# Optimization experiments

Measured on AMD Instinct MI355X. Metric: run time of the kernel, lower is better.

Reference implementation:

```python
import jax, jax.numpy as jnp
import numpy as np

D_NIBBLE = 16
NIBBLE_VALUES = 16
NUM_NIBBLES = 8


def _build_tables():
    num_entries = NIBBLE_VALUES * NIBBLE_VALUES * 2  # 512
    input_dim = 2 * D_NIBBLE + 2                     # 34
    W1 = np.zeros((input_dim, num_entries), dtype=np.float32)
    W2_sum = np.zeros((num_entries, D_NIBBLE), dtype=np.float32)
    W2_carry = np.zeros((num_entries, 2), dtype=np.float32)
    for a in range(NIBBLE_VALUES):
        for b in range(NIBBLE_VALUES):
            for c in range(2):
                k = a * 32 + b * 2 + c
                W1[a, k] = 1.0
                W1[D_NIBBLE + b, k] = 1.0
                W1[2 * D_NIBBLE + c, k] = 1.0
                total = a + b + c
                W2_sum[k, total % 16] = 1.0
                W2_carry[k, 1 if total >= 16 else 0] = 1.0
    return jnp.asarray(W1), jnp.asarray(W2_sum), jnp.asarray(W2_carry)


def setup_inputs() -> dict:
    key = jax.random.key(0)
    k1, k2 = jax.random.split(key)
    B = 32768
    a_nibbles = jax.random.uniform(k1, (B, NUM_NIBBLES, 32), dtype=jnp.float32)
    b_nibbles = jax.random.uniform(k2, (B, NUM_NIBBLES, 32), dtype=jnp.float32)
    W1, W2_sum, W2_carry = _build_tables()
    threshold = jnp.float32(2.5)
    return {"a_nibbles": a_nibbles, "b_nibbles": b_nibbles,
            "W1": W1, "W2_sum": W2_sum, "W2_carry": W2_carry,
            "threshold": threshold}


def reference(a_nibbles, b_nibbles, W1, W2_sum, W2_carry, threshold):
    # a_nibbles, b_nibbles: [B, 8, 32]; first 16 feats = value one-hot, rest = pos
    B = a_nibbles.shape[0]
    carry0 = jnp.zeros((B, 2), a_nibbles.dtype).at[:, 0].set(1.0)  # carry=0 one-hot
    a_steps = jnp.swapaxes(a_nibbles, 0, 1)  # [8, B, 32]
    b_steps = jnp.swapaxes(b_nibbles, 0, 1)

    def step(carry, ab):
        a, b = ab  # [B, 32] each
        x = jnp.concatenate([a[:, :D_NIBBLE], b[:, :D_NIBBLE], carry], axis=-1)  # [B,34]
        scores = x @ W1                                     # [B,512]
        weights = jax.nn.softmax((scores - threshold) * 10.0, axis=-1)
        result = weights @ W2_sum                           # [B,16]
        new_carry = weights @ W2_carry                      # [B,2]
        out = jnp.concatenate([result, a[:, D_NIBBLE:]], axis=-1)  # [B,32]
        return new_carry, out

    _, outs = jax.lax.scan(step, carry0, (a_steps, b_steps))  # outs: [8, B, 32]
    return jnp.swapaxes(outs, 0, 1)  # [B, 8, 32]
```

## Files before the change

### kernel.cpp

```cpp
#include <hip/hip_runtime.h>


#define LOG2E10 14.426950408889634f

#if __has_builtin(__builtin_amdgcn_exp2f)
#define EXP2F(x) __builtin_amdgcn_exp2f(x)
#else
#define EXP2F(x) exp2f(x)
#endif

#if __has_builtin(__builtin_amdgcn_rcpf)
#define RCPF(x) __builtin_amdgcn_rcpf(x)
#else
#define RCPF(x) (1.0f / (x))
#endif

#define EBZ(x) ebz[(x) + 12]

template <int CTRL>
__device__ __forceinline__ float qdpp(float x) {
    return __int_as_float(__builtin_amdgcn_update_dpp(
        0, __float_as_int(x), CTRL, 0xF, 0xF, true));
}

__global__ __launch_bounds__(256, 2) void AdditionFFN_kernel(
    const float4* __restrict__ A, const float4* __restrict__ Bv,
    float4* __restrict__ O, int nRows)
{
    const int T = threadIdx.x;
    const int c = T & 3;
    const int row = blockIdx.x * 64 + (T >> 2);
    if (row >= nRows) return;
    const float4* a4 = A + (size_t)row * 64;
    const float4* b4 = Bv + (size_t)row * 64;
    float4* o4 = O + (size_t)row * 64;

    float4 AV[8], BV[8], PV[8];
    #pragma unroll
    for (int s = 0; s < 8; ++s) {
        AV[s] = a4[s * 8 + c];
        BV[s] = b4[s * 8 + c];
        PV[s] = a4[s * 8 + 4 + c];
    }

    float ec0 = EXP2F(LOG2E10);
    float ec1 = 1.0f;

    #pragma unroll
    for (int s = 0; s < 8; ++s) {
        o4[s * 8 + 4 + c] = PV[s];

        const float4 av = AV[s], bv = BV[s];

        float ea_own[4] = { EXP2F(av.x * LOG2E10), EXP2F(av.y * LOG2E10),
                            EXP2F(av.z * LOG2E10), EXP2F(av.w * LOG2E10) };
        float eb_own[4] = { EXP2F(bv.x * LOG2E10), EXP2F(bv.y * LOG2E10),
                            EXP2F(bv.z * LOG2E10), EXP2F(bv.w * LOG2E10) };

        float ea[16];
        #pragma unroll
        for (int m = 0; m < 4; ++m) {
            ea[m]      = qdpp<0x00>(ea_own[m]);
            ea[4 + m]  = qdpp<0x55>(ea_own[m]);
            ea[8 + m]  = qdpp<0xAA>(ea_own[m]);
            ea[12 + m] = qdpp<0xFF>(ea_own[m]);
        }

        float ebr[4][4];
        #pragma unroll
        for (int m = 0; m < 4; ++m) {
            ebr[0][m] = eb_own[m];
            ebr[1][m] = qdpp<0x39>(eb_own[m]);
            ebr[2][m] = qdpp<0x4E>(eb_own[m]);
            ebr[3][m] = qdpp<0x93>(eb_own[m]);
        }

        float ebz[28];
        #pragma unroll
        for (int x = -12; x <= 15; ++x) {
            float vsh = ebr[(x >> 2) & 3][x & 3];
            bool keep;
            if (x >= 0 && x <= 3)  keep = true;
            else if (x < 0)        keep = (c >= ((3 - x) >> 2));
            else                   keep = (c <= ((15 - x) >> 2));
            EBZ(x) = keep ? vsh : 0.0f;
        }

        float ulo[5], uhi[5];
        #pragma unroll
        for (int i = 0; i < 5; ++i) {
            float acc = 0.0f;
            const int amax = (i + 11 < 15) ? (i + 11) : 15;
            #pragma unroll
            for (int a = 0; a <= amax; ++a) {
                acc = __builtin_fmaf(ea[a], EBZ(i - 1 - a), acc);
            }
            ulo[i] = acc;
        }
        #pragma unroll
        for (int i = 0; i < 5; ++i) {
            float acc = 0.0f;
            #pragma unroll
            for (int a = i; a < 16; ++a) {
                acc = __builtin_fmaf(ea[a], EBZ(i + 15 - a), acc);
            }
            uhi[i] = acc;
        }

        float sap = (ea_own[0] + ea_own[1]) + (ea_own[2] + ea_own[3]);
        sap += qdpp<0xB1>(sap);
        sap += qdpp<0x4E>(sap);
        float sbp = (eb_own[0] + eb_own[1]) + (eb_own[2] + eb_own[3]);
        sbp += qdpp<0xB1>(sbp);
        sbp += qdpp<0x4E>(sbp);
        const float E = ec0 + ec1;
        float Z = sap * sbp * E;
        float rZ = RCPF(Z);
        rZ = rZ * (2.0f - Z * rZ);

        float hi0p = (uhi[1] + uhi[2]) + (uhi[3] + uhi[4]);
        float phi = hi0p * E + ((c == 0) ? uhi[0] * ec1 : 0.0f);
        phi += qdpp<0xB1>(phi);
        phi += qdpp<0x4E>(phi);
        float carry1 = phi * rZ;
#if __has_builtin(__builtin_amdgcn_fmed3f)
        carry1 = __builtin_amdgcn_fmed3f(carry1, 0.0f, 1.0f);
#else
        carry1 = fminf(fmaxf(carry1, 0.0f), 1.0f);
#endif
        float carry0 = 1.0f - carry1;

        float vm1 = ulo[0] + uhi[0];
        float v0 = ulo[1] + uhi[1];
        float v1 = ulo[2] + uhi[2];
        float v2 = ulo[3] + uhi[3];
        float v3 = ulo[4] + uhi[4];
        float4 r;
        r.x = (v0 * ec0 + vm1 * ec1) * rZ;
        r.y = (v1 * ec0 + v0 * ec1) * rZ;
        r.z = (v2 * ec0 + v1 * ec1) * rZ;
        r.w = (v3 * ec0 + v2 * ec1) * rZ;
        o4[s * 8 + c] = r;

        ec0 = EXP2F(carry0 * LOG2E10);
        ec1 = EXP2F(carry1 * LOG2E10);
    }
}

extern "C" void kernel_launch(void* const* d_in, const int* in_sizes, int n_in,
                              void* d_out, int out_size, void* d_ws, size_t ws_size,
                              hipStream_t stream) {
    (void)n_in; (void)out_size; (void)d_ws; (void)ws_size;
    const int nRows = in_sizes[0] / 256;
    const float4* A  = (const float4*)d_in[0];
    const float4* Bv = (const float4*)d_in[1];
    float4* O = (float4*)d_out;
    int blocks = (nRows + 63) / 64;
    AdditionFFN_kernel<<<blocks, 256, 0, stream>>>(A, Bv, O, nRows);
}
```

Measured before the change: 112.8 us.

## Parallelize nibble steps across lanes, resolve carry chain with scalar scan

```diff
diff --git a/kernel.cpp b/kernel.cpp
--- a/kernel.cpp
+++ b/kernel.cpp
@@ -23,128 +23,144 @@
         0, __float_as_int(x), CTRL, 0xF, 0xF, true));
 }
 
-__global__ __launch_bounds__(256, 2) void AdditionFFN_kernel(
+template <int OFF>
+__device__ __forceinline__ float swz32(float x) {
+    return __int_as_float(__builtin_amdgcn_ds_swizzle(__float_as_int(x), OFF));
+}
+
+__global__ __launch_bounds__(256, 4) void AdditionFFN_kernel(
     const float4* __restrict__ A, const float4* __restrict__ Bv,
     float4* __restrict__ O, int nRows)
 {
     const int T = threadIdx.x;
-    const int c = T & 3;
-    const int row = blockIdx.x * 64 + (T >> 2);
+    const int r = T & 31;
+    const int c = r & 3;
+    const int s = r >> 2;
+    const int row = blockIdx.x * 8 + (T >> 5);
     if (row >= nRows) return;
     const float4* a4 = A + (size_t)row * 64;
     const float4* b4 = Bv + (size_t)row * 64;
     float4* o4 = O + (size_t)row * 64;
 
-    float4 AV[8], BV[8], PV[8];
+    const float4 av = a4[s * 8 + c];
+    const float4 bv = b4[s * 8 + c];
+    const float4 pv = a4[s * 8 + 4 + c];
+    o4[s * 8 + 4 + c] = pv;
+
+    float ea_own[4] = { EXP2F(av.x * LOG2E10), EXP2F(av.y * LOG2E10),
+                        EXP2F(av.z * LOG2E10), EXP2F(av.w * LOG2E10) };
+    float eb_own[4] = { EXP2F(bv.x * LOG2E10), EXP2F(bv.y * LOG2E10),
+                        EXP2F(bv.z * LOG2E10), EXP2F(bv.w * LOG2E10) };
+
+    float ea[16];
     #pragma unroll
-    for (int s = 0; s < 8; ++s) {
-        AV[s] = a4[s * 8 + c];
-        BV[s] = b4[s * 8 + c];
-        PV[s] = a4[s * 8 + 4 + c];
+    for (int m = 0; m < 4; ++m) {
+        ea[m]      = qdpp<0x00>(ea_own[m]);
+        ea[4 + m]  = qdpp<0x55>(ea_own[m]);
+        ea[8 + m]  = qdpp<0xAA>(ea_own[m]);
+        ea[12 + m] = qdpp<0xFF>(ea_own[m]);
     }
 
-    float ec0 = EXP2F(LOG2E10);
-    float ec1 = 1.0f;
+    float ebr[4][4];
+    #pragma unroll
+    for (int m = 0; m < 4; ++m) {
+        ebr[0][m] = eb_own[m];
+        ebr[1][m] = qdpp<0x39>(eb_own[m]);
+        ebr[2][m] = qdpp<0x4E>(eb_own[m]);
+        ebr[3][m] = qdpp<0x93>(eb_own[m]);
+    }
 
+    float ebz[28];
     #pragma unroll
-    for (int s = 0; s < 8; ++s) {
-        o4[s * 8 + 4 + c] = PV[s];
+    for (int x = -12; x <= 15; ++x) {
+        float vsh = ebr[(x >> 2) & 3][x & 3];
+        bool keep;
+        if (x >= 0 && x <= 3)  keep = true;
+        else if (x < 0)        keep = (c >= ((3 - x) >> 2));
+        else                   keep = (c <= ((15 - x) >> 2));
+        EBZ(x) = keep ? vsh : 0.0f;
+    }
 
-        const float4 av = AV[s], bv = BV[s];
+    float ulo[5], uhi[5];
+    #pragma unroll
+    for (int i = 0; i < 5; ++i) {
+        float acc = 0.0f;
+        const int amax = (i + 11 < 15) ? (i + 11) : 15;
+        #pragma unroll
+        for (int a = 0; a <= amax; ++a) {
+            acc = __builtin_fmaf(ea[a], EBZ(i - 1 - a), acc);
+        }
+        ulo[i] = acc;
+    }
+    #pragma unroll
+    for (int i = 0; i < 5; ++i) {
+        float acc = 0.0f;
+        #pragma unroll
+        for (int a = i; a < 16; ++a) {
+            acc = __builtin_fmaf(ea[a], EBZ(i + 15 - a), acc);
+        }
+        uhi[i] = acc;
+    }
 
-        float ea_own[4] = { EXP2F(av.x * LOG2E10), EXP2F(av.y * LOG2E10),
-                            EXP2F(av.z * LOG2E10), EXP2F(av.w * LOG2E10) };
-        float eb_own[4] = { EXP2F(bv.x * LOG2E10), EXP2F(bv.y * LOG2E10),
-                            EXP2F(bv.z * LOG2E10), EXP2F(bv.w * LOG2E10) };
+    float sap = (ea_own[0] + ea_own[1]) + (ea_own[2] + ea_own[3]);
+    sap += qdpp<0xB1>(sap);
+    sap += qdpp<0x4E>(sap);
+    float sbp = (eb_own[0] + eb_own[1]) + (eb_own[2] + eb_own[3]);
+    sbp += qdpp<0xB1>(sbp);
+    sbp += qdpp<0x4E>(sbp);
+    float Nm = sap * sbp;
+    float rN = RCPF(Nm);
+    rN = rN * (2.0f - Nm * rN);
 
-        float ea[16];
-        #pragma unroll
-        for (int m = 0; m < 4; ++m) {
-            ea[m]      = qdpp<0x00>(ea_own[m]);
-            ea[4 + m]  = qdpp<0x55>(ea_own[m]);
-            ea[8 + m]  = qdpp<0xAA>(ea_own[m]);
-            ea[12 + m] = qdpp<0xFF>(ea_own[m]);
-        }
+    float hi0p = (uhi[1] + uhi[2]) + (uhi[3] + uhi[4]);
+    hi0p += qdpp<0xB1>(hi0p);
+    hi0p += qdpp<0x4E>(hi0p);
+    float hs = hi0p * rN;
+    float ms = qdpp<0x00>(uhi[0]) * rN;
 
-        float ebr[4][4];
-        #pragma unroll
-        for (int m = 0; m < 4; ++m) {
-            ebr[0][m] = eb_own[m];
-            ebr[1][m] = qdpp<0x39>(eb_own[m]);
-            ebr[2][m] = qdpp<0x4E>(eb_own[m]);
-            ebr[3][m] = qdpp<0x93>(eb_own[m]);
-        }
+    float h0 = swz32<0x003>(hs), m0 = swz32<0x003>(ms);
+    float h1 = swz32<0x083>(hs), m1 = swz32<0x083>(ms);
+    float h2 = swz32<0x103>(hs), m2 = swz32<0x103>(ms);
+    float h3 = swz32<0x183>(hs), m3 = swz32<0x183>(ms);
+    float h4 = swz32<0x203>(hs), m4 = swz32<0x203>(ms);
+    float h5 = swz32<0x283>(hs), m5 = swz32<0x283>(ms);
+    float h6 = swz32<0x303>(hs), m6 = swz32<0x303>(ms);
+    float h7 = swz32<0x383>(hs), m7 = swz32<0x383>(ms);
 
-        float ebz[28];
-        #pragma unroll
-        for (int x = -12; x <= 15; ++x) {
-            float vsh = ebr[(x >> 2) & 3][x & 3];
-            bool keep;
-            if (x >= 0 && x <= 3)  keep = true;
-            else if (x < 0)        keep = (c >= ((3 - x) >> 2));
-            else                   keep = (c <= ((15 - x) >> 2));
-            EBZ(x) = keep ? vsh : 0.0f;
-        }
+    float c1 = 0.0f, wmine = 0.0f;
+#define CARRY_STEP(K, HK, MK)                                        \
+    {                                                                \
+        float e0 = EXP2F((1.0f - c1) * LOG2E10);                     \
+        float e1 = EXP2F(c1 * LOG2E10);                              \
+        float E = e0 + e1;                                           \
+        float rE = RCPF(E);                                          \
+        rE = rE * (2.0f - E * rE);                                   \
+        float w = e1 * rE;                                           \
+        if (s == K) wmine = w;                                       \
+        c1 = __builtin_fmaf(w, MK, HK);                              \
+        c1 = fminf(fmaxf(c1, 0.0f), 1.0f);                           \
+    }
+    CARRY_STEP(0, h0, m0)
+    CARRY_STEP(1, h1, m1)
+    CARRY_STEP(2, h2, m2)
+    CARRY_STEP(3, h3, m3)
+    CARRY_STEP(4, h4, m4)
+    CARRY_STEP(5, h5, m5)
+    CARRY_STEP(6, h6, m6)
+    CARRY_STEP(7, h7, m7)
+#undef CARRY_STEP
 
-        float ulo[5], uhi[5];
-        #pragma unroll
-        for (int i = 0; i < 5; ++i) {
-            float acc = 0.0f;
-            const int amax = (i + 11 < 15) ? (i + 11) : 15;
-            #pragma unroll
-            for (int a = 0; a <= amax; ++a) {
-                acc = __builtin_fmaf(ea[a], EBZ(i - 1 - a), acc);
-            }
-            ulo[i] = acc;
-        }
-        #pragma unroll
-        for (int i = 0; i < 5; ++i) {
-            float acc = 0.0f;
-            #pragma unroll
-            for (int a = i; a < 16; ++a) {
-                acc = __builtin_fmaf(ea[a], EBZ(i + 15 - a), acc);
-            }
-            uhi[i] = acc;
-        }
-
-        float sap = (ea_own[0] + ea_own[1]) + (ea_own[2] + ea_own[3]);
-        sap += qdpp<0xB1>(sap);
-        sap += qdpp<0x4E>(sap);
-        float sbp = (eb_own[0] + eb_own[1]) + (eb_own[2] + eb_own[3]);
-        sbp += qdpp<0xB1>(sbp);
-        sbp += qdpp<0x4E>(sbp);
-        const float E = ec0 + ec1;
-        float Z = sap * sbp * E;
-        float rZ = RCPF(Z);
-        rZ = rZ * (2.0f - Z * rZ);
-
-        float hi0p = (uhi[1] + uhi[2]) + (uhi[3] + uhi[4]);
-        float phi = hi0p * E + ((c == 0) ? uhi[0] * ec1 : 0.0f);
-        phi += qdpp<0xB1>(phi);
-        phi += qdpp<0x4E>(phi);
-        float carry1 = phi * rZ;
-#if __has_builtin(__builtin_amdgcn_fmed3f)
-        carry1 = __builtin_amdgcn_fmed3f(carry1, 0.0f, 1.0f);
-#else
-        carry1 = fminf(fmaxf(carry1, 0.0f), 1.0f);
-#endif
-        float carry0 = 1.0f - carry1;
-
-        float vm1 = ulo[0] + uhi[0];
-        float v0 = ulo[1] + uhi[1];
-        float v1 = ulo[2] + uhi[2];
-        float v2 = ulo[3] + uhi[3];
-        float v3 = ulo[4] + uhi[4];
-        float4 r;
-        r.x = (v0 * ec0 + vm1 * ec1) * rZ;
-        r.y = (v1 * ec0 + v0 * ec1) * rZ;
-        r.z = (v2 * ec0 + v1 * ec1) * rZ;
-        r.w = (v3 * ec0 + v2 * ec1) * rZ;
-        o4[s * 8 + c] = r;
-
-        ec0 = EXP2F(carry0 * LOG2E10);
-        ec1 = EXP2F(carry1 * LOG2E10);
-    }
+    float vm1 = ulo[0] + uhi[0];
+    float v0 = ulo[1] + uhi[1];
+    float v1 = ulo[2] + uhi[2];
+    float v2 = ulo[3] + uhi[3];
+    float v3 = ulo[4] + uhi[4];
+    float4 rr;
+    rr.x = __builtin_fmaf(wmine, vm1 - v0, v0) * rN;
+    rr.y = __builtin_fmaf(wmine, v0 - v1, v1) * rN;
+    rr.z = __builtin_fmaf(wmine, v1 - v2, v2) * rN;
+    rr.w = __builtin_fmaf(wmine, v2 - v3, v3) * rN;
+    o4[s * 8 + c] = rr;
 }
 
 extern "C" void kernel_launch(void* const* d_in, const int* in_sizes, int n_in,
@@ -155,6 +171,6 @@
     const float4* A  = (const float4*)d_in[0];
     const float4* Bv = (const float4*)d_in[1];
     float4* O = (float4*)d_out;
-    int blocks = (nRows + 63) / 64;
+    int blocks = (nRows + 7) / 8;
     AdditionFFN_kernel<<<blocks, 256, 0, stream>>>(A, Bv, O, nRows);
 }
```

Measured after the change: 109.5 us. 1.03x faster.
